# Optimization experiments

Measured on AMD Instinct MI355X. Metric: run time of the kernel, lower is better.

## Reference

```python
import jax, jax.numpy as jnp
import numpy as np


def setup_inputs() -> dict:
    key = jax.random.key(0)
    k1, k2, k3, k4 = jax.random.split(key, 4)
    B, F, E = 8, 64, 50000
    Cout, K = 128, 5
    x = jax.random.normal(k1, (B, F, E), dtype=jnp.float32)
    gemm = jax.random.randint(k2, (B, E, 4), 0, E, dtype=jnp.int64)  # 1-ring neighbor edge indices
    fan_in = F * K
    W = jax.random.normal(k3, (Cout, F, 1, K), dtype=jnp.float32) / np.sqrt(fan_in)
    b = jax.random.normal(k4, (Cout,), dtype=jnp.float32) * 0.01
    return {"x": x, "gemm": gemm, "W": W, "b": b}


def reference(x, gemm, W, b):
    # x: [B, F, E] edge features; gemm: [B, E, 4] neighbor indices in [0, E)
    B, F, E = x.shape
    # pad_gemm prepends the edge's own index as column 0; create_gemm shifts by +1
    # and pads x with a zero column at index 0 (slot for missing / -1 neighbors).
    xp = jnp.concatenate([jnp.zeros((B, F, 1), dtype=x.dtype), x], axis=2)  # [B, F, E+1]
    self_idx = jnp.broadcast_to(jnp.arange(E, dtype=gemm.dtype)[None, :, None], (B, E, 1))
    idx = jnp.concatenate([self_idx, gemm], axis=2) + 1  # [B, E, 5], indices into E+1 slots
    # gather: f[b, f, e, k] = xp[b, f, idx[b, e, k]]
    xp_t = jnp.transpose(xp, (0, 2, 1))  # [B, E+1, F]
    f = jnp.take_along_axis(xp_t, idx.reshape(B, E * 5, 1), axis=1)  # [B, E*5, F]
    f = jnp.transpose(f.reshape(B, E, 5, F), (0, 3, 1, 2))  # [B, F, E, 5]
    # symmetric (order-invariant) pooling over the 4 neighbors
    x0 = f[:, :, :, 0]
    x1 = f[:, :, :, 1] + f[:, :, :, 3]
    x2 = f[:, :, :, 2] + f[:, :, :, 4]
    x3 = jnp.abs(f[:, :, :, 1] - f[:, :, :, 3])
    x4 = jnp.abs(f[:, :, :, 2] - f[:, :, :, 4])
    G = jnp.stack([x0, x1, x2, x3, x4], axis=3)  # [B, F, E, 5]
    # Conv2d with kernel (1, 5) over width-5 map == contraction over (F, 5)
    out = jnp.einsum('bfek,ofk->boe', G, W[:, :, 0, :]) + b[None, :, None]
    return out[..., None]  # [B, Cout, E, 1]
```

## Files before the change

kernel.cpp:

```cpp
#include <hip/hip_runtime.h>
#include <hip/hip_bf16.h>

#define NB 8
#define NF 64
#define NE 50000
#define NO 128
#define NK 320
#define CONV_GRID 768

typedef short short8 __attribute__((ext_vector_type(8)));
typedef float f32x4 __attribute__((ext_vector_type(4)));

__device__ __forceinline__ unsigned short f2bf(float x) {
    union { float f; unsigned int u; } v; v.f = x;
    unsigned int r = v.u + 0x7fffu + ((v.u >> 16) & 1u);
    return (unsigned short)(r >> 16);
}
__device__ __forceinline__ float bf2f(unsigned short h) {
    union { unsigned int u; float f; } v; v.u = ((unsigned int)h) << 16; return v.f;
}

__global__ __launch_bounds__(256) void transpose_x(
    const float* __restrict__ x, unsigned short* __restrict__ xT, int E)
{
    __shared__ float tile[64][65];
    int ntiles = (E + 63) >> 6;
    int b = blockIdx.x / ntiles;
    int t = blockIdx.x % ntiles;
    int e0 = t << 6;
    int le = threadIdx.x & 63;
    int q  = threadIdx.x >> 6;
    const float* xb = x + (size_t)b * NF * E;
    #pragma unroll
    for (int i = 0; i < 16; ++i) {
        int f = q * 16 + i;
        int e = e0 + le;
        tile[f][le] = (e < E) ? xb[(size_t)f * E + e] : 0.0f;
    }
    __syncthreads();
    unsigned short* xTb = xT + (size_t)b * E * NF;
    int fp = (threadIdx.x & 31) * 2;
    int es = threadIdx.x >> 5;
    #pragma unroll
    for (int i = 0; i < 8; ++i) {
        int el = i * 8 + es;
        int e = e0 + el;
        if (e < E) {
            unsigned int pk = (unsigned int)f2bf(tile[fp][el])
                            | ((unsigned int)f2bf(tile[fp + 1][el]) << 16);
            *(unsigned int*)&xTb[(size_t)e * NF + fp] = pk;
        }
    }
}

__global__ __launch_bounds__(256) void prep_w(
    const float* __restrict__ W, unsigned short* __restrict__ Wt)
{
    int idx = blockIdx.x * 256 + threadIdx.x;
    if (idx >= NK * NO) return;
    int K = idx >> 7;
    int o = idx & 127;
    int f  = K & 63;
    int kp = K >> 6;
    float v = W[(size_t)o * (NF * 5) + f * 5 + kp];
    Wt[((size_t)(K >> 3) * NO + o) * 8 + (K & 7)] = f2bf(v);
}

__global__ __launch_bounds__(256) void conv_main(
    const unsigned short* __restrict__ xT,
    const int* __restrict__ gemm,
    const unsigned short* __restrict__ Wt,
    const float* __restrict__ bias,
    float* __restrict__ out,
    int E)
{
    __shared__ __align__(16) unsigned short Gs[40 * 64 * 8];

    int tid  = threadIdx.x;
    int wave = tid >> 6;
    int lane = tid & 63;
    int l16  = lane & 15;
    int lq   = lane >> 4;

    short8 wfrag[10][2];
    #pragma unroll
    for (int ks = 0; ks < 10; ++ks)
        #pragma unroll
        for (int m = 0; m < 2; ++m) {
            int o = (wave * 2 + m) * 16 + l16;
            wfrag[ks][m] = *(const short8*)&Wt[((size_t)(ks * 4 + lq) * NO + o) * 8];
        }
    float biasr[2][4];
    #pragma unroll
    for (int m = 0; m < 2; ++m)
        #pragma unroll
        for (int r = 0; r < 4; ++r)
            biasr[m][r] = bias[(wave * 2 + m) * 16 + lq * 4 + r];

    int ntiles = (E + 63) >> 6;
    int nunits = NB * ntiles;
    int ge = tid >> 2;
    int j  = tid & 3;

    for (int unit = blockIdx.x; unit < nunits; unit += gridDim.x) {
        int b     = unit / ntiles;
        int etile = unit % ntiles;

        {
            int e  = etile * 64 + ge;
            int eC = (e < E) ? e : (E - 1);
            const unsigned short* xb = xT + (size_t)b * E * NF;
            int4 gv = *(const int4*)(gemm + ((size_t)b * E + eC) * 4);
            int gi[5];
            gi[0] = eC; gi[1] = gv.x; gi[2] = gv.y; gi[3] = gv.z; gi[4] = gv.w;

            #pragma unroll
            for (int half = 0; half < 2; ++half) {
                int f0 = half * 32 + j * 8;
                uint4 craw[5];
                #pragma unroll
                for (int k = 0; k < 5; ++k)
                    craw[k] = *(const uint4*)&xb[(size_t)gi[k] * NF + f0];

                const unsigned short* c1 = (const unsigned short*)&craw[1];
                const unsigned short* c2 = (const unsigned short*)&craw[2];
                const unsigned short* c3 = (const unsigned short*)&craw[3];
                const unsigned short* c4 = (const unsigned short*)&craw[4];

                uint4 pk[5];
                pk[0] = craw[0];
                unsigned short gb[4][8];
                #pragma unroll
                for (int i = 0; i < 8; ++i) {
                    float a1 = bf2f(c1[i]), a2 = bf2f(c2[i]);
                    float a3 = bf2f(c3[i]), a4 = bf2f(c4[i]);
                    gb[0][i] = f2bf(a1 + a3);
                    gb[1][i] = f2bf(a2 + a4);
                    gb[2][i] = f2bf(fabsf(a1 - a3));
                    gb[3][i] = f2bf(fabsf(a2 - a4));
                }
                pk[1] = *(uint4*)&gb[0][0];
                pk[2] = *(uint4*)&gb[1][0];
                pk[3] = *(uint4*)&gb[2][0];
                pk[4] = *(uint4*)&gb[3][0];

                #pragma unroll
                for (int kp = 0; kp < 5; ++kp) {
                    int kblk = kp * 8 + half * 4 + j;
                    *(uint4*)&Gs[((size_t)kblk * 64 + ge) * 8] = pk[kp];
                }
            }
        }
        __syncthreads();

        f32x4 acc[2][4];
        #pragma unroll
        for (int m = 0; m < 2; ++m)
            #pragma unroll
            for (int nt = 0; nt < 4; ++nt)
                acc[m][nt] = (f32x4){0.f, 0.f, 0.f, 0.f};

        #pragma unroll
        for (int ks = 0; ks < 10; ++ks) {
            short8 bb[4];
            #pragma unroll
            for (int nt = 0; nt < 4; ++nt)
                bb[nt] = *(const short8*)&Gs[(((size_t)(ks * 4 + lq)) * 64 + nt * 16 + l16) * 8];
            #pragma unroll
            for (int m = 0; m < 2; ++m)
                #pragma unroll
                for (int nt = 0; nt < 4; ++nt)
                    acc[m][nt] = __builtin_amdgcn_mfma_f32_16x16x32_bf16(
                        wfrag[ks][m], bb[nt], acc[m][nt], 0, 0, 0);
        }

        int e0 = etile * 64;
        #pragma unroll
        for (int m = 0; m < 2; ++m) {
            #pragma unroll
            for (int nt = 0; nt < 4; ++nt) {
                int e = e0 + nt * 16 + l16;
                if (e < E) {
                    #pragma unroll
                    for (int r = 0; r < 4; ++r) {
                        int o = (wave * 2 + m) * 16 + lq * 4 + r;
                        out[((size_t)b * NO + o) * E + e] = acc[m][nt][r] + biasr[m][r];
                    }
                }
            }
        }
        __syncthreads();
    }
}

extern "C" void kernel_launch(void* const* d_in, const int* in_sizes, int n_in,
                              void* d_out, int out_size, void* d_ws, size_t ws_size,
                              hipStream_t stream)
{
    const float* x    = (const float*)d_in[0];
    const int*   gemm = (const int*)d_in[1];
    const float* W    = (const float*)d_in[2];
    const float* bias = (const float*)d_in[3];
    float* out = (float*)d_out;

    const int E = NE;
    unsigned short* Wt = (unsigned short*)d_ws;
    unsigned short* xT = (unsigned short*)((char*)d_ws + 131072);

    prep_w<<<(NK * NO + 255) / 256, 256, 0, stream>>>(W, Wt);

    int ntiles = (E + 63) / 64;
    transpose_x<<<NB * ntiles, 256, 0, stream>>>(x, xT, E);

    conv_main<<<CONV_GRID, 256, 0, stream>>>(xT, gemm, Wt, bias, out, E);
}
```

Before: 371.3 us.

## Prefetch next tile's gathers across MFMA phase and vectorize output stores

Software-pipelines the persistent conv loop. The neighbor gathers and gemm indices for the next tile are loaded into registers before the current tile's MFMA work, so gather latency overlaps compute. The MFMA operands are swapped so each lane holds 4 consecutive edges, which lets the output be written as 16-byte vector stores instead of scalar stores. The grid shrinks to 512 blocks and launch bounds request 2 blocks per CU, at the cost of more register pressure from the prefetch buffers.

```diff
diff --git a/kernel.cpp b/kernel.cpp
--- a/kernel.cpp
+++ b/kernel.cpp
@@ -6,7 +6,7 @@
 #define NE 50000
 #define NO 128
 #define NK 320
-#define CONV_GRID 768
+#define CONV_GRID 512
 
 typedef short short8 __attribute__((ext_vector_type(8)));
 typedef float f32x4 __attribute__((ext_vector_type(4)));
@@ -66,7 +66,7 @@
     Wt[((size_t)(K >> 3) * NO + o) * 8 + (K & 7)] = f2bf(v);
 }
 
-__global__ __launch_bounds__(256) void conv_main(
+__global__ __launch_bounds__(256, 2) void conv_main(
     const unsigned short* __restrict__ xT,
     const int* __restrict__ gemm,
     const unsigned short* __restrict__ Wt,
@@ -86,106 +86,131 @@
     #pragma unroll
     for (int ks = 0; ks < 10; ++ks)
         #pragma unroll
-        for (int m = 0; m < 2; ++m) {
-            int o = (wave * 2 + m) * 16 + l16;
-            wfrag[ks][m] = *(const short8*)&Wt[((size_t)(ks * 4 + lq) * NO + o) * 8];
-        }
-    float biasr[2][4];
-    #pragma unroll
-    for (int m = 0; m < 2; ++m)
-        #pragma unroll
-        for (int r = 0; r < 4; ++r)
-            biasr[m][r] = bias[(wave * 2 + m) * 16 + lq * 4 + r];
+        for (int ot = 0; ot < 2; ++ot) {
+            int o = (wave * 2 + ot) * 16 + l16;
+            wfrag[ks][ot] = *(const short8*)&Wt[((size_t)(ks * 4 + lq) * NO + o) * 8];
+        }
+    float biasv[2];
+    #pragma unroll
+    for (int ot = 0; ot < 2; ++ot)
+        biasv[ot] = bias[(wave * 2 + ot) * 16 + l16];
 
     int ntiles = (E + 63) >> 6;
     int nunits = NB * ntiles;
     int ge = tid >> 2;
     int j  = tid & 3;
-
-    for (int unit = blockIdx.x; unit < nunits; unit += gridDim.x) {
-        int b     = unit / ntiles;
-        int etile = unit % ntiles;
+    int step = gridDim.x;
+
+    if (blockIdx.x >= nunits) return;
+
+    uint4 craw[2][5];
+    int4  gvn;
+
+    {
+        int u = blockIdx.x;
+        int b = u / ntiles, et = u % ntiles;
+        int e = et * 64 + ge; int eC = (e < E) ? e : (E - 1);
+        int4 gv = *(const int4*)(gemm + ((size_t)b * E + eC) * 4);
+        const unsigned short* xb = xT + (size_t)b * E * NF;
+        int gi[5]; gi[0] = eC; gi[1] = gv.x; gi[2] = gv.y; gi[3] = gv.z; gi[4] = gv.w;
+        #pragma unroll
+        for (int half = 0; half < 2; ++half) {
+            int f0 = half * 32 + j * 8;
+            #pragma unroll
+            for (int k = 0; k < 5; ++k)
+                craw[half][k] = *(const uint4*)&xb[(size_t)gi[k] * NF + f0];
+        }
+        int un = u + step; if (un > nunits - 1) un = nunits - 1;
+        int bn = un / ntiles, etn = un % ntiles;
+        int en = etn * 64 + ge; int eCn = (en < E) ? en : (E - 1);
+        gvn = *(const int4*)(gemm + ((size_t)bn * E + eCn) * 4);
+    }
+
+    for (int u = blockIdx.x; u < nunits; u += step) {
+        int b = u / ntiles, etile = u % ntiles;
+
+        #pragma unroll
+        for (int half = 0; half < 2; ++half) {
+            const unsigned short* c1 = (const unsigned short*)&craw[half][1];
+            const unsigned short* c2 = (const unsigned short*)&craw[half][2];
+            const unsigned short* c3 = (const unsigned short*)&craw[half][3];
+            const unsigned short* c4 = (const unsigned short*)&craw[half][4];
+            uint4 pk[5];
+            pk[0] = craw[half][0];
+            unsigned short gb[4][8];
+            #pragma unroll
+            for (int i = 0; i < 8; ++i) {
+                float a1 = bf2f(c1[i]), a2 = bf2f(c2[i]);
+                float a3 = bf2f(c3[i]), a4 = bf2f(c4[i]);
+                gb[0][i] = f2bf(a1 + a3);
+                gb[1][i] = f2bf(a2 + a4);
+                gb[2][i] = f2bf(fabsf(a1 - a3));
+                gb[3][i] = f2bf(fabsf(a2 - a4));
+            }
+            pk[1] = *(uint4*)&gb[0][0];
+            pk[2] = *(uint4*)&gb[1][0];
+            pk[3] = *(uint4*)&gb[2][0];
+            pk[4] = *(uint4*)&gb[3][0];
+            #pragma unroll
+            for (int kp = 0; kp < 5; ++kp) {
+                int kblk = kp * 8 + half * 4 + j;
+                *(uint4*)&Gs[((size_t)kblk * 64 + ge) * 8] = pk[kp];
+            }
+        }
+        __syncthreads();
 
         {
-            int e  = etile * 64 + ge;
-            int eC = (e < E) ? e : (E - 1);
-            const unsigned short* xb = xT + (size_t)b * E * NF;
-            int4 gv = *(const int4*)(gemm + ((size_t)b * E + eC) * 4);
-            int gi[5];
-            gi[0] = eC; gi[1] = gv.x; gi[2] = gv.y; gi[3] = gv.z; gi[4] = gv.w;
-
+            int un = u + step; if (un > nunits - 1) un = nunits - 1;
+            int bn = un / ntiles, etn = un % ntiles;
+            const unsigned short* xbn = xT + (size_t)bn * E * NF;
+            int en = etn * 64 + ge; int eCn = (en < E) ? en : (E - 1);
+            int gi[5]; gi[0] = eCn; gi[1] = gvn.x; gi[2] = gvn.y; gi[3] = gvn.z; gi[4] = gvn.w;
             #pragma unroll
             for (int half = 0; half < 2; ++half) {
                 int f0 = half * 32 + j * 8;
-                uint4 craw[5];
                 #pragma unroll
                 for (int k = 0; k < 5; ++k)
-                    craw[k] = *(const uint4*)&xb[(size_t)gi[k] * NF + f0];
-
-                const unsigned short* c1 = (const unsigned short*)&craw[1];
-                const unsigned short* c2 = (const unsigned short*)&craw[2];
-                const unsigned short* c3 = (const unsigned short*)&craw[3];
-                const unsigned short* c4 = (const unsigned short*)&craw[4];
-
-                uint4 pk[5];
-                pk[0] = craw[0];
-                unsigned short gb[4][8];
-                #pragma unroll
-                for (int i = 0; i < 8; ++i) {
-                    float a1 = bf2f(c1[i]), a2 = bf2f(c2[i]);
-                    float a3 = bf2f(c3[i]), a4 = bf2f(c4[i]);
-                    gb[0][i] = f2bf(a1 + a3);
-                    gb[1][i] = f2bf(a2 + a4);
-                    gb[2][i] = f2bf(fabsf(a1 - a3));
-                    gb[3][i] = f2bf(fabsf(a2 - a4));
-                }
-                pk[1] = *(uint4*)&gb[0][0];
-                pk[2] = *(uint4*)&gb[1][0];
-                pk[3] = *(uint4*)&gb[2][0];
-                pk[4] = *(uint4*)&gb[3][0];
-
-                #pragma unroll
-                for (int kp = 0; kp < 5; ++kp) {
-                    int kblk = kp * 8 + half * 4 + j;
-                    *(uint4*)&Gs[((size_t)kblk * 64 + ge) * 8] = pk[kp];
-                }
-            }
-        }
-        __syncthreads();
-
-        f32x4 acc[2][4];
-        #pragma unroll
-        for (int m = 0; m < 2; ++m)
-            #pragma unroll
-            for (int nt = 0; nt < 4; ++nt)
-                acc[m][nt] = (f32x4){0.f, 0.f, 0.f, 0.f};
+                    craw[half][k] = *(const uint4*)&xbn[(size_t)gi[k] * NF + f0];
+            }
+            int un2 = un + step; if (un2 > nunits - 1) un2 = nunits - 1;
+            int bn2 = un2 / ntiles, etn2 = un2 % ntiles;
+            int en2 = etn2 * 64 + ge; int eC2 = (en2 < E) ? en2 : (E - 1);
+            gvn = *(const int4*)(gemm + ((size_t)bn2 * E + eC2) * 4);
+        }
+
+        f32x4 acc[4][2];
+        #pragma unroll
+        for (int et = 0; et < 4; ++et)
+            #pragma unroll
+            for (int ot = 0; ot < 2; ++ot)
+                acc[et][ot] = (f32x4){0.f, 0.f, 0.f, 0.f};
 
         #pragma unroll
         for (int ks = 0; ks < 10; ++ks) {
             short8 bb[4];
             #pragma unroll
-            for (int nt = 0; nt < 4; ++nt)
-                bb[nt] = *(const short8*)&Gs[(((size_t)(ks * 4 + lq)) * 64 + nt * 16 + l16) * 8];
-            #pragma unroll
-            for (int m = 0; m < 2; ++m)
+            for (int et = 0; et < 4; ++et)
+                bb[et] = *(const short8*)&Gs[(((size_t)(ks * 4 + lq)) * 64 + et * 16 + l16) * 8];
+            #pragma unroll
+            for (int et = 0; et < 4; ++et)
                 #pragma unroll
-                for (int nt = 0; nt < 4; ++nt)
-                    acc[m][nt] = __builtin_amdgcn_mfma_f32_16x16x32_bf16(
-                        wfrag[ks][m], bb[nt], acc[m][nt], 0, 0, 0);
+                for (int ot = 0; ot < 2; ++ot)
+                    acc[et][ot] = __builtin_amdgcn_mfma_f32_16x16x32_bf16(
+                        bb[et], wfrag[ks][ot], acc[et][ot], 0, 0, 0);
         }
 
         int e0 = etile * 64;
         #pragma unroll
-        for (int m = 0; m < 2; ++m) {
-            #pragma unroll
-            for (int nt = 0; nt < 4; ++nt) {
-                int e = e0 + nt * 16 + l16;
-                if (e < E) {
-                    #pragma unroll
-                    for (int r = 0; r < 4; ++r) {
-                        int o = (wave * 2 + m) * 16 + lq * 4 + r;
-                        out[((size_t)b * NO + o) * E + e] = acc[m][nt][r] + biasr[m][r];
-                    }
+        for (int et = 0; et < 4; ++et) {
+            int eb = e0 + et * 16 + lq * 4;
+            if (eb < E) {
+                #pragma unroll
+                for (int ot = 0; ot < 2; ++ot) {
+                    int o = (wave * 2 + ot) * 16 + l16;
+                    f32x4 v = acc[et][ot];
+                    float bv = biasv[ot];
+                    v[0] += bv; v[1] += bv; v[2] += bv; v[3] += bv;
+                    *(f32x4*)&out[((size_t)b * NO + o) * E + eb] = v;
                 }
             }
         }
```

After: 370.6 us. Within noise of the previous version (-0.2%).
